# Kernel tuning notes

Measured on AMD Instinct MI355X. Metric: run time of the kernel, lower is better.

The kernel has to match this reference:

```python
import jax, jax.numpy as jnp
import numpy as np

D_STATE = 16
D_CONV = 4


def _ln_cf(x, w, b, eps=1e-6):
    # channels_first LayerNorm over dim 1 of (B,C,H,W)
    u = x.mean(1, keepdims=True)
    s = ((x - u) ** 2).mean(1, keepdims=True)
    return w[:, None, None] * ((x - u) / jnp.sqrt(s + eps)) + b[:, None, None]


def _ln_last(x, w, b, eps=1e-5):
    u = x.mean(-1, keepdims=True)
    s = ((x - u) ** 2).mean(-1, keepdims=True)
    return (x - u) / jnp.sqrt(s + eps) * w + b


def _mamba(xn, Win, convw, convb, Wx, Wdt, bdt, Alog, Dp):
    # xn: (B, L, d_model); returns (B, L, d_inner) (out_proj is Identity in this module)
    B, L, _ = xn.shape
    di = Win.shape[0] // 2
    xz = xn @ Win.T                                   # (B,L,2*di), in_proj bias=False
    xc, z = xz[..., :di], xz[..., di:]
    # causal depthwise conv1d along L (pad left d_conv-1, slice == torch pad+trim)
    xt = jnp.pad(xc.transpose(0, 2, 1), ((0, 0), (0, 0), (D_CONV - 1, 0)))
    xt = jax.lax.conv_general_dilated(xt, convw[:, None, :], (1,), 'VALID',
                                      dimension_numbers=('NCH', 'OIH', 'NCH'),
                                      feature_group_count=di)
    xs = jax.nn.silu(xt + convb[None, :, None]).transpose(0, 2, 1)  # (B,L,di)
    dtr = Wdt.shape[1]
    x_dbl = xs @ Wx.T                                 # (B,L,dtr+2*ds)
    dt = x_dbl[..., :dtr]
    Bm = x_dbl[..., dtr:dtr + D_STATE]                # (B,L,ds)
    Cm = x_dbl[..., dtr + D_STATE:]                   # (B,L,ds)
    delta = jax.nn.softplus(dt @ Wdt.T + bdt)         # (B,L,di)
    A = -jnp.exp(Alog)                                # (di,ds)
    dA = jnp.exp(delta[..., None] * A)                # (B,L,di,ds)
    dBx = delta[..., None] * Bm[:, :, None, :] * xs[..., None]

    def step(h, ab):
        a, b2 = ab
        h = a * h + b2
        return h, h

    h0 = jnp.zeros((B, di, D_STATE), xn.dtype)
    _, hs = jax.lax.scan(step, h0, (dA.transpose(1, 0, 2, 3), dBx.transpose(1, 0, 2, 3)))
    y = jnp.einsum('lbds,bls->bld', hs, Cm) + xs * Dp
    return y * jax.nn.silu(z)


def _dwconv2d(u, k, dil):
    c = k.shape[0]
    return jax.lax.conv_general_dilated(u, k[:, None], (1, 1),
                                        [(dil, dil), (dil, dil)],
                                        rhs_dilation=(dil, dil),
                                        dimension_numbers=('NCHW', 'OIHW', 'NCHW'),
                                        feature_group_count=c)


def _block(x, gamma1, gamma2, ln1_w, ln1_b, mn_w, mn_b,
           f_Win, f_convw, f_convb, f_Wx, f_Wdt, f_bdt, f_Alog, f_D,
           b_Win, b_convw, b_convb, b_Wx, b_Wdt, b_bdt, b_Alog, b_D,
           Wout, msff_win, msff_dw1, msff_dw2, msff_dw3, msff_wout):
    B, C, H, W = x.shape
    L = H * W
    # --- BiPixelMambaLayer branch ---
    x1 = _ln_cf(x, ln1_w, ln1_b)                       # norm1 (channels_first)
    xf = x1.reshape(B, C, L).transpose(0, 2, 1)        # (B,L,C)
    xn = _ln_last(xf, mn_w, mn_b)                      # inner nn.LayerNorm (eps=1e-5)
    yf = _mamba(xn, f_Win, f_convw, f_convb, f_Wx, f_Wdt, f_bdt, f_Alog, f_D)
    yb = _mamba(xn[:, ::-1], b_Win, b_convw, b_convb, b_Wx, b_Wdt, b_bdt, b_Alog, b_D)
    yo = (yf + yb[:, ::-1]) @ Wout.T                   # shared out_proj (bias=False)
    x = x + gamma1[:, None, None] * (yo.transpose(0, 2, 1).reshape(B, C, H, W) + x1)
    # --- MSFF branch (norm1 reused) ---
    inp = x
    xm = _ln_cf(x, ln1_w, ln1_b)
    h = jnp.einsum('oc,bchw->bohw', msff_win, xm)      # project_in (1x1x1 conv, depth=1)
    hid = msff_dw1.shape[0]
    h1 = _dwconv2d(h[:, :hid], msff_dw1, 1)            # Conv3d 3x3x3 w/ depth=1 == 2D center slice
    h2 = _dwconv2d(h[:, hid:2 * hid], msff_dw2, 2)
    h3 = _dwconv2d(h[:, 2 * hid:], msff_dw3, 3)
    g = jax.nn.gelu(h1, approximate=False) * h2 * h3
    xm = jnp.einsum('oc,bchw->bohw', msff_wout, g)     # project_out
    return inp + gamma2[:, None, None] * xm


def setup_inputs() -> dict:
    key = jax.random.key(0)
    ks = jax.random.split(key, 40)
    dim, di, dtr, ds, hid, Bn, H, W = 96, 192, 6, 16, 192, 2, 64, 64
    r = lambda i, shape, s=0.05: jax.random.normal(ks[i], shape, jnp.float32) * s
    inp = {
        'x': r(0, (Bn, dim, H, W), 1.0),
        'gamma1': r(1, (dim,), 0.1), 'gamma2': r(2, (dim,), 0.1),
        'ln1_w': 1.0 + r(3, (dim,), 0.1), 'ln1_b': r(4, (dim,), 0.1),
        'mn_w': 1.0 + r(5, (dim,), 0.1), 'mn_b': r(6, (dim,), 0.1),
    }
    i = 7
    for p in ('f_', 'b_'):
        inp[p + 'Win'] = r(i, (2 * di, dim)); i += 1
        inp[p + 'convw'] = r(i, (di, D_CONV), 0.2); i += 1
        inp[p + 'convb'] = r(i, (di,), 0.1); i += 1
        inp[p + 'Wx'] = r(i, (dtr + 2 * ds, di)); i += 1
        inp[p + 'Wdt'] = r(i, (di, dtr), 0.1); i += 1
        inp[p + 'bdt'] = r(i, (di,), 0.1); i += 1
        inp[p + 'Alog'] = jax.random.uniform(ks[i], (di, ds), jnp.float32, 0.0, 2.5); i += 1
        inp[p + 'D'] = r(i, (di,), 0.5); i += 1
    inp['Wout'] = r(i, (dim, di)); i += 1
    inp['msff_win'] = r(i, (3 * hid, dim)); i += 1
    inp['msff_dw1'] = r(i, (hid, 3, 3), 0.2); i += 1
    inp['msff_dw2'] = r(i, (hid, 3, 3), 0.2); i += 1
    inp['msff_dw3'] = r(i, (hid, 3, 3), 0.2); i += 1
    inp['msff_wout'] = r(i, (dim, hid)); i += 1
    return inp


def reference(x, gamma1, gamma2, ln1_w, ln1_b, mn_w, mn_b,
              f_Win, f_convw, f_convb, f_Wx, f_Wdt, f_bdt, f_Alog, f_D,
              b_Win, b_convw, b_convb, b_Wx, b_Wdt, b_bdt, b_Alog, b_D,
              Wout, msff_win, msff_dw1, msff_dw2, msff_dw3, msff_wout):
    return _block(x, gamma1, gamma2, ln1_w, ln1_b, mn_w, mn_b,
                  f_Win, f_convw, f_convb, f_Wx, f_Wdt, f_bdt, f_Alog, f_D,
                  b_Win, b_convw, b_convb, b_Wx, b_Wdt, b_bdt, b_Alog, b_D,
                  Wout, msff_win, msff_dw1, msff_dw2, msff_dw3, msff_wout)
```

## Files before the change

### kernel.cpp

```cpp
#include <hip/hip_runtime.h>
#include <hip/hip_bf16.h>
#include <math.h>

typedef __hip_bfloat16 bf16;
typedef _Float16 f16;
typedef f16  f16x8  __attribute__((ext_vector_type(8)));
typedef short short8 __attribute__((ext_vector_type(8)));
typedef unsigned short ushort8 __attribute__((ext_vector_type(8)));
typedef float floatx4 __attribute__((ext_vector_type(4)));

#define L_SEQ 4096
#define BATCH 2
#define DIM   96
#define DI    192
#define DS    16
#define HID   192
#define NPOS  (BATCH * L_SEQ)
#define NCH   256
#define CHUNK 16
#define GRP   16
#define NGRP  (NCH / GRP)
#define NREC  (2 * BATCH * DI)
#define LDBL  40
#define PLANE (4 * NCH * DI * 8)
#define LOG2E 1.44269504088896f
#define TP    32

__device__ __forceinline__ float silu_f(float x) { return x / (1.f + __expf(-x)); }
__device__ __forceinline__ float softplus_f(float x) {
    return fmaxf(x, 0.f) + __logf(1.f + __expf(-fabsf(x)));
}
__device__ __forceinline__ float b2f(bf16 v) { return __bfloat162float(v); }
__device__ __forceinline__ float us2f(unsigned short u) {
    union { unsigned int i; float f; } cv; cv.i = ((unsigned int)u) << 16; return cv.f;
}

__global__ void k_ln12_prep(const float* __restrict__ x,
                            const float* __restrict__ ln1w, const float* __restrict__ ln1b,
                            const float* __restrict__ mnw,  const float* __restrict__ mnb,
                            bf16* __restrict__ XNbf,
                            const float* __restrict__ fWin, const float* __restrict__ bWin,
                            const float* __restrict__ fWx,  const float* __restrict__ bWx,
                            const float* __restrict__ Wout, const float* __restrict__ mwin,
                            const float* __restrict__ mwout,
                            const float* __restrict__ fAlog, const float* __restrict__ bAlog,
                            const float* __restrict__ mdw1, const float* __restrict__ mdw2,
                            const float* __restrict__ mdw3,
                            bf16* __restrict__ war, float* __restrict__ a2tab,
                            float* __restrict__ mdwt) {
    __shared__ float xt[DIM][TP + 1];
    __shared__ float rs[8][TP], rss[8][TP];
    __shared__ float uu[TP], rr[TP];
    if (blockIdx.x >= NPOS / TP) {
        int i = (blockIdx.x - NPOS / TP) * 256 + threadIdx.x;
        if (i < 180480) {
            float v;
            if (i < 36864)        v = fWin[i];
            else if (i < 73728)   v = bWin[i - 36864];
            else if (i < 81024)   v = fWx[i - 73728];
            else if (i < 88320)   v = bWx[i - 81024];
            else if (i < 106752)  v = Wout[i - 88320];
            else if (i < 162048)  v = mwin[i - 106752];
            else                  v = mwout[i - 162048];
            war[i] = __float2bfloat16(v);
        } else if (i < 186624) {
            int j = i - 180480;
            int dirq = j / 3072, rem = j % 3072;
            const float* al = dirq ? bAlog : fAlog;
            a2tab[j] = -__expf(al[rem]) * LOG2E;
        } else if (i < 191808) {
            int j = i - 186624;
            int cv = j / 1728, rem = j % 1728;
            int tap = rem / 192, c = rem % 192;
            const float* src = (cv == 0) ? mdw1 : (cv == 1) ? mdw2 : mdw3;
            mdwt[j] = src[c * 9 + tap];
        }
        return;
    }
    int p0 = blockIdx.x * TP;
    int b = p0 >> 12, l0 = p0 & (L_SEQ - 1);
    int t = threadIdx.x;
    int tg = t >> 5, li = t & 31;

    for (int idx = t; idx < DIM * TP; idx += 256) {
        int c = idx >> 5, q = idx & 31;
        xt[c][q] = x[((size_t)(b * DIM + c)) * L_SEQ + l0 + q];
    }
    __syncthreads();
    {
        float s = 0.f, ss = 0.f;
        for (int c = tg; c < DIM; c += 8) { float v = xt[c][li]; s += v; ss += v * v; }
        rs[tg][li] = s; rss[tg][li] = ss;
    }
    __syncthreads();
    if (t < TP) {
        float s = 0.f, ss = 0.f;
#pragma unroll
        for (int g = 0; g < 8; g++) { s += rs[g][t]; ss += rss[g][t]; }
        float u = s / DIM;
        uu[t] = u; rr[t] = rsqrtf(ss / DIM - u * u + 1e-6f);
    }
    __syncthreads();
    {
        float u = uu[li], r = rr[li];
        float s2 = 0.f, ss2 = 0.f;
        for (int c = tg; c < DIM; c += 8) {
            float tv = ln1w[c] * (xt[c][li] - u) * r + ln1b[c];
            xt[c][li] = tv;
            s2 += tv; ss2 += tv * tv;
        }
        rs[tg][li] = s2; rss[tg][li] = ss2;
    }
    __syncthreads();
    if (t < TP) {
        float s = 0.f, ss = 0.f;
#pragma unroll
        for (int g = 0; g < 8; g++) { s += rs[g][t]; ss += rss[g][t]; }
        float u = s / DIM;
        uu[t] = u; rr[t] = rsqrtf(ss / DIM - u * u + 1e-5f);
    }
    __syncthreads();
    for (int idx = t; idx < DIM * TP; idx += 256) {
        int q = idx / DIM, c = idx % DIM;
        XNbf[(size_t)(p0 + q) * DIM + c] =
            __float2bfloat16((xt[c][q] - uu[q]) * rr[q] * mnw[c] + mnb[c]);
    }
}

__global__ void mfma_nt_dir(const bf16* __restrict__ A0, const bf16* __restrict__ A1,
                            const bf16* __restrict__ W0, const bf16* __restrict__ W1,
                            void* __restrict__ C0, void* __restrict__ C1,
                            int M, int N, int K, int ldc, int pad6, int obf) {
    int z = blockIdx.z;
    const bf16* A = z ? A1 : A0;
    const bf16* W = z ? W1 : W0;
    void* C = z ? C1 : C0;
    int wave = threadIdx.x >> 6, lane = threadIdx.x & 63;
    int m0 = blockIdx.x * 64 + wave * 16;
    int n0 = blockIdx.y * 64;
    int lm = lane & 15, quad = lane >> 4;
    const short* Ap = (const short*)A + (size_t)(m0 + lm) * K + quad * 8;
    const short* Wp = (const short*)W;
    floatx4 acc[4];
#pragma unroll
    for (int t = 0; t < 4; t++) acc[t] = (floatx4){0.f, 0.f, 0.f, 0.f};
    for (int k0 = 0; k0 < K; k0 += 32) {
        short8 a = *(const short8*)(Ap + k0);
#pragma unroll
        for (int t = 0; t < 4; t++) {
            int n = n0 + t * 16 + lm;
            short8 b = (n < N) ? *(const short8*)(Wp + (size_t)n * K + k0 + quad * 8)
                               : (short8){0,0,0,0,0,0,0,0};
            acc[t] = __builtin_amdgcn_mfma_f32_16x16x32_bf16(a, b, acc[t], 0, 0, 0);
        }
    }
#pragma unroll
    for (int t = 0; t < 4; t++) {
        int n = n0 + t * 16 + lm;
        if (n < N) {
            int nn = (pad6 && n >= 6) ? n + 2 : n;
#pragma unroll
            for (int r = 0; r < 4; r++) {
                int m = m0 + quad * 4 + r;
                if (obf) ((bf16*)C)[(size_t)m * ldc + nn] = __float2bfloat16(acc[t][r]);
                else     ((float*)C)[(size_t)m * ldc + nn] = acc[t][r];
            }
        }
    }
}

__global__ void k_conv_dbl(const bf16* __restrict__ XZF, const bf16* __restrict__ XZB,
                           const float* __restrict__ fw, const float* __restrict__ fb,
                           const float* __restrict__ bw, const float* __restrict__ bb,
                           const bf16* __restrict__ fWxB, const bf16* __restrict__ bWxB,
                           float* __restrict__ DBLF, float* __restrict__ DBLB,
                           bf16* __restrict__ XSF, bf16* __restrict__ XSB) {
    __shared__ __align__(16) unsigned short xs_t[64][200];
    int dirb = blockIdx.y;
    int p0 = blockIdx.x * 64;
    const bf16* XZ = dirb ? XZB : XZF;
    const float* cw = dirb ? bw : fw;
    const float* cb = dirb ? bb : fb;
    bf16* XS = dirb ? XSB : XSF;

    for (int u = threadIdx.x; u < 64 * 24; u += 256) {
        int dg = u % 24, pl = u / 24;
        int p = p0 + pl;
        int b = p >> 12, l = p & (L_SEQ - 1);
        int d0 = dg * 8;
        float4 w[8];
#pragma unroll
        for (int j = 0; j < 8; j++) w[j] = *(const float4*)(cw + (d0 + j) * 4);
        float acc[8];
#pragma unroll
        for (int j = 0; j < 8; j++) acc[j] = cb[d0 + j];
#pragma unroll
        for (int k = 0; k < 4; k++) {
            int ls = dirb ? (l + 3 - k) : (l - 3 + k);
            if (ls >= 0 && ls < L_SEQ) {
                ushort8 xv = *(const ushort8*)((const unsigned short*)XZ +
                               ((size_t)(b * L_SEQ + ls)) * 384 + d0);
#pragma unroll
                for (int j = 0; j < 8; j++) {
                    float wk = (k == 0) ? w[j].x : (k == 1) ? w[j].y : (k == 2) ? w[j].z : w[j].w;
                    acc[j] += wk * us2f(xv[j]);
                }
            }
        }
        ushort8 ov;
#pragma unroll
        for (int j = 0; j < 8; j++) {
            bf16 tv = __float2bfloat16(silu_f(acc[j]));
            ov[j] = *(unsigned short*)&tv;
        }
        *(ushort8*)((unsigned short*)XS + (size_t)p * DI + d0) = ov;
        *(ushort8*)&xs_t[pl][d0] = ov;
    }
    __syncthreads();
    int t = threadIdx.x;
    int w = t >> 6, lane = t & 63;
    int lm = lane & 15, quad = lane >> 4;
    const bf16* Wx = dirb ? bWxB : fWxB;
    float* DBL = dirb ? DBLB : DBLF;
    floatx4 acc[3];
#pragma unroll
    for (int tt = 0; tt < 3; tt++) acc[tt] = (floatx4){0.f, 0.f, 0.f, 0.f};
    const unsigned short* ar = &xs_t[w * 16 + lm][0];
#pragma unroll
    for (int k = 0; k < 6; k++) {
        int k0 = k * 32 + quad * 8;
        short8 a = *(const short8*)(ar + k0);
#pragma unroll
        for (int tt = 0; tt < 3; tt++) {
            int n = tt * 16 + lm;
            short8 bq = (n < 38) ? *(const short8*)((const short*)Wx + n * 192 + k0)
                                 : (short8){0,0,0,0,0,0,0,0};
            acc[tt] = __builtin_amdgcn_mfma_f32_16x16x32_bf16(a, bq, acc[tt], 0, 0, 0);
        }
    }
#pragma unroll
    for (int tt = 0; tt < 3; tt++) {
        int n = tt * 16 + lm;
        if (n < 38) {
            int nn = (n >= 6) ? n + 2 : n;
#pragma unroll
            for (int r = 0; r < 4; r++) {
                int m = p0 + w * 16 + quad * 4 + r;
                DBL[(size_t)m * LDBL + nn] = acc[tt][r];
            }
        }
    }
}

__global__ void k_scan_p1g(const float* __restrict__ DBLF, const float* __restrict__ DBLB,
                           const bf16* __restrict__ XSF,  const bf16* __restrict__ XSB,
                           const float* __restrict__ fWdt, const float* __restrict__ fbdt,
                           const float* __restrict__ bWdt, const float* __restrict__ bbdt,
                           const float* __restrict__ a2tab,
                           f16* __restrict__ Pexc, f16* __restrict__ Qexc,
                           float* __restrict__ Pg, float* __restrict__ Qg) {
    __shared__ f16x8 Pl[2][GRP][16];
    __shared__ f16x8 Ql[2][GRP][16];
    int dsl = blockIdx.x, grp = blockIdx.y, dirb = blockIdx.z;
    int t = threadIdx.x;
    int chunk = t >> 4, dl = t & 15;
    int d = dsl * 16 + dl;
    int b = dirb & 1, dir = dirb >> 1;
    int gc = grp * GRP + chunk;

    const float* DBL = dir ? DBLB : DBLF;
    const bf16*  XS  = dir ? XSB  : XSF;
    const float* wdt = (dir ? bWdt : fWdt) + d * 6;
    float bdtv = (dir ? bbdt : fbdt)[d];

    float wd[6];
#pragma unroll
    for (int r = 0; r < 6; r++) wd[r] = wdt[r];
    const float* a2p = a2tab + (dir * DI + d) * 16;
    float A2[16], h[16];
#pragma unroll
    for (int v = 0; v < 4; v++) {
        float4 a2v = *(const float4*)(a2p + 4 * v);
        A2[4*v] = a2v.x; A2[4*v+1] = a2v.y; A2[4*v+2] = a2v.z; A2[4*v+3] = a2v.w;
    }
#pragma unroll
    for (int s = 0; s < 16; s++) h[s] = 0.f;

    int l = dir ? (L_SEQ - 1 - gc * CHUNK) : gc * CHUNK;
    int stp = dir ? -1 : 1;
    float sumdel = 0.f;

    for (int i = 0; i < CHUNK; i++) {
        size_t p = (size_t)b * L_SEQ + l;
        const float* row = DBL + p * LDBL;
        float dtv = bdtv;
#pragma unroll
        for (int r = 0; r < 6; r++) dtv += row[r] * wd[r];
        float del = softplus_f(dtv);
        float xs  = b2f(XS[p * DI + d]);
        const float4* bm = (const float4*)(row + 8);
        float4 B0 = bm[0], B1 = bm[1], B2 = bm[2], B3 = bm[3];
        float Bm[16] = {B0.x,B0.y,B0.z,B0.w, B1.x,B1.y,B1.z,B1.w,
                        B2.x,B2.y,B2.z,B2.w, B3.x,B3.y,B3.z,B3.w};
        float dx = del * xs;
        sumdel += del;
#pragma unroll
        for (int s = 0; s < 16; s++) {
            float dA = exp2f(del * A2[s]);
            h[s] = dA * h[s] + dx * Bm[s];
        }
        l += stp;
    }
    {
        f16x8 p0, p1, q0, q1;
#pragma unroll
        for (int j = 0; j < 8; j++) {
            q0[j] = (f16)h[j];
            q1[j] = (f16)h[8 + j];
            p0[j] = (f16)exp2f(A2[j] * sumdel);
            p1[j] = (f16)exp2f(A2[8 + j] * sumdel);
        }
        Pl[0][chunk][dl] = p0; Pl[1][chunk][dl] = p1;
        Ql[0][chunk][dl] = q0; Ql[1][chunk][dl] = q1;
    }
    __syncthreads();

    {
        int s  = t & 15, dl2 = t >> 4;
        int s8 = s >> 3, sl = s & 7;
        f16* Pp = (f16*)&Pl[s8][0][dl2];
        f16* Qp = (f16*)&Ql[s8][0][dl2];
        float runP = 1.f, runQ = 0.f;
#pragma unroll
        for (int c = 0; c < GRP; c++) {
            float pv = (float)Pp[c * 128 + sl];
            float qv = (float)Qp[c * 128 + sl];
            Pp[c * 128 + sl] = (f16)runP;
            Qp[c * 128 + sl] = (f16)runQ;
            runQ = pv * runQ + qv;
            runP *= pv;
        }
        int d2 = dsl * 16 + dl2;
        size_t gidx = (((size_t)(dirb * NGRP + grp)) * DI + d2) * 16 + s;
        Pg[gidx] = runP;
        Qg[gidx] = runQ;
    }
    __syncthreads();

    {
        size_t base = ((size_t)(dirb * NCH + gc) * DI + d) * 8;
        *(f16x8*)(Pexc + base)         = Pl[0][chunk][dl];
        *(f16x8*)(Pexc + PLANE + base) = Pl[1][chunk][dl];
        *(f16x8*)(Qexc + base)         = Ql[0][chunk][dl];
        *(f16x8*)(Qexc + PLANE + base) = Ql[1][chunk][dl];
    }
}

__global__ void k_scan_p3g(const float* __restrict__ DBLF, const float* __restrict__ DBLB,
                           const bf16* __restrict__ XSF,  const bf16* __restrict__ XSB,
                           const bf16* __restrict__ XZF,  const bf16* __restrict__ XZB,
                           const float* __restrict__ fWdt, const float* __restrict__ fbdt,
                           const float* __restrict__ bWdt, const float* __restrict__ bbdt,
                           const float* __restrict__ a2tab,
                           const float* __restrict__ fD,    const float* __restrict__ bD,
                           const f16* __restrict__ Pexc, const f16* __restrict__ Qexc,
                           const float* __restrict__ Pg, const float* __restrict__ Qg,
                           bf16* __restrict__ YSF, bf16* __restrict__ YSB) {
    __shared__ float qx[16][17];
    int dsl = blockIdx.x, grp = blockIdx.y, dirb = blockIdx.z;
    int t = threadIdx.x;
    {
        int dl = t >> 4, s = t & 15;
        int d2 = dsl * 16 + dl;
        float runQ = 0.f;
        for (int g = 0; g < grp; g++) {
            size_t i = (((size_t)(dirb * NGRP + g)) * DI + d2) * 16 + s;
            runQ = Pg[i] * runQ + Qg[i];
        }
        qx[dl][s] = runQ;
    }
    __syncthreads();

    int chunk = t >> 4, dl = t & 15;
    int d = dsl * 16 + dl;
    int gc = grp * GRP + chunk;
    int b = dirb & 1, dir = dirb >> 1;

    const float* DBL = dir ? DBLB : DBLF;
    const bf16*  XS  = dir ? XSB  : XSF;
    const bf16*  XZ  = dir ? XZB  : XZF;
    const float* wdt = (dir ? bWdt : fWdt) + d * 6;
    float bdtv = (dir ? bbdt : fbdt)[d];
    float Dp = dir ? bD[d] : fD[d];
    bf16* Y = dir ? YSB : YSF;

    float wd[6];
#pragma unroll
    for (int r = 0; r < 6; r++) wd[r] = wdt[r];
    const float* a2p = a2tab + (dir * DI + d) * 16;
    float A2[16], h[16];
#pragma unroll
    for (int v = 0; v < 4; v++) {
        float4 a2v = *(const float4*)(a2p + 4 * v);
        A2[4*v] = a2v.x; A2[4*v+1] = a2v.y; A2[4*v+2] = a2v.z; A2[4*v+3] = a2v.w;
    }
    {
        size_t base = ((size_t)(dirb * NCH + gc) * DI + d) * 8;
        f16x8 pe0 = *(const f16x8*)(Pexc + base);
        f16x8 pe1 = *(const f16x8*)(Pexc + PLANE + base);
        f16x8 qe0 = *(const f16x8*)(Qexc + base);
        f16x8 qe1 = *(const f16x8*)(Qexc + PLANE + base);
#pragma unroll
        for (int j = 0; j < 8; j++) {
            h[j]     = (float)pe0[j] * qx[dl][j]     + (float)qe0[j];
            h[8 + j] = (float)pe1[j] * qx[dl][8 + j] + (float)qe1[j];
        }
    }

    int l = dir ? (L_SEQ - 1 - gc * CHUNK) : gc * CHUNK;
    int stp = dir ? -1 : 1;

    for (int i = 0; i < CHUNK; i++) {
        size_t p = (size_t)b * L_SEQ + l;
        const float* row = DBL + p * LDBL;
        float dtv = bdtv;
#pragma unroll
        for (int r = 0; r < 6; r++) dtv += row[r] * wd[r];
        float del = softplus_f(dtv);
        float xs  = b2f(XS[p * DI + d]);
        float z   = b2f(XZ[p * 384 + 192 + d]);
        const float4* bm = (const float4*)(row + 8);
        float4 B0 = bm[0], B1 = bm[1], B2 = bm[2], B3 = bm[3];
        float4 C0 = bm[4], C1 = bm[5], C2 = bm[6], C3 = bm[7];
        float Bm[16] = {B0.x,B0.y,B0.z,B0.w, B1.x,B1.y,B1.z,B1.w,
                        B2.x,B2.y,B2.z,B2.w, B3.x,B3.y,B3.z,B3.w};
        float Cm[16] = {C0.x,C0.y,C0.z,C0.w, C1.x,C1.y,C1.z,C1.w,
                        C2.x,C2.y,C2.z,C2.w, C3.x,C3.y,C3.z,C3.w};
        float dx = del * xs;
        float pr = 0.f;
#pragma unroll
        for (int s = 0; s < 16; s++) {
            float dA = exp2f(del * A2[s]);
            h[s] = dA * h[s] + dx * Bm[s];
            pr += h[s] * Cm[s];
        }
        Y[p * DI + d] = __float2bfloat16((pr + xs * Dp) * silu_f(z));
        l += stp;
    }
}

__global__ void k_out_mid(const bf16* __restrict__ Y1, const bf16* __restrict__ Y2,
                          const bf16* __restrict__ W,
                          const float* __restrict__ x, const float* __restrict__ gamma1,
                          const float* __restrict__ ln1w, const float* __restrict__ ln1b,
                          const bf16* __restrict__ mwinB,
                          float* __restrict__ XMID, bf16* __restrict__ H) {
    __shared__ float yt[DIM][TP + 1];
    __shared__ float xt[DIM][TP + 1];
    __shared__ float rs[8][TP], rss[8][TP];
    __shared__ float uu[TP], rr[TP];
    __shared__ __align__(16) unsigned short xmt[TP][104];
    int p0 = blockIdx.x * TP;
    int b = p0 >> 12, l0 = p0 & (L_SEQ - 1);
    int t = threadIdx.x;
    int tg = t >> 5, li = t & 31;

    {
        int w = t >> 6, lane = t & 63;
        int lm = lane & 15, quad = lane >> 4;
        int mh = w & 1, nb = (w >> 1) * 3;
        const short* A1p = (const short*)Y1 + (size_t)(p0 + mh * 16 + lm) * 192 + quad * 8;
        const short* A2p = (const short*)Y2 + (size_t)(p0 + mh * 16 + lm) * 192 + quad * 8;
        const short* Wp  = (const short*)W;
        floatx4 acc[3];
#pragma unroll
        for (int tt = 0; tt < 3; tt++) acc[tt] = (floatx4){0.f, 0.f, 0.f, 0.f};
#pragma unroll
        for (int k = 0; k < 6; k++) {
            int k0 = k * 32;
            short8 a1 = *(const short8*)(A1p + k0);
            short8 a2 = *(const short8*)(A2p + k0);
#pragma unroll
            for (int tt = 0; tt < 3; tt++) {
                int n = (nb + tt) * 16 + lm;
                short8 bq = *(const short8*)(Wp + (size_t)n * 192 + k0 + quad * 8);
                acc[tt] = __builtin_amdgcn_mfma_f32_16x16x32_bf16(a1, bq, acc[tt], 0, 0, 0);
                acc[tt] = __builtin_amdgcn_mfma_f32_16x16x32_bf16(a2, bq, acc[tt], 0, 0, 0);
            }
        }
#pragma unroll
        for (int tt = 0; tt < 3; tt++) {
            int c = (nb + tt) * 16 + lm;
#pragma unroll
            for (int r = 0; r < 4; r++)
                yt[c][mh * 16 + quad * 4 + r] = acc[tt][r];
        }
    }
    for (int idx = t; idx < DIM * TP; idx += 256) {
        int c = idx >> 5, q = idx & 31;
        xt[c][q] = x[((size_t)(b * DIM + c)) * L_SEQ + l0 + q];
    }
    __syncthreads();
    {
        float s = 0.f, ss = 0.f;
        for (int c = tg; c < DIM; c += 8) { float v = xt[c][li]; s += v; ss += v * v; }
        rs[tg][li] = s; rss[tg][li] = ss;
    }
    __syncthreads();
    if (t < TP) {
        float s = 0.f, ss = 0.f;
#pragma unroll
        for (int g = 0; g < 8; g++) { s += rs[g][t]; ss += rss[g][t]; }
        float u = s / DIM;
        uu[t] = u; rr[t] = rsqrtf(ss / DIM - u * u + 1e-6f);
    }
    __syncthreads();
    {
        float u = uu[li], r = rr[li];
        float s = 0.f, ss = 0.f;
        for (int c = tg; c < DIM; c += 8) {
            float xv = xt[c][li];
            float x1 = ln1w[c] * (xv - u) * r + ln1b[c];
            float v = xv + gamma1[c] * (yt[c][li] + x1);
            XMID[((size_t)(b * DIM + c)) * L_SEQ + l0 + li] = v;
            xt[c][li] = v;
            s += v; ss += v * v;
        }
        rs[tg][li] = s; rss[tg][li] = ss;
    }
    __syncthreads();
    if (t < TP) {
        float s = 0.f, ss = 0.f;
#pragma unroll
        for (int g = 0; g < 8; g++) { s += rs[g][t]; ss += rss[g][t]; }
        float u = s / DIM;
        uu[t] = u; rr[t] = rsqrtf(ss / DIM - u * u + 1e-6f);
    }
    __syncthreads();
    for (int idx = t; idx < DIM * TP; idx += 256) {
        int q = idx / DIM, c = idx % DIM;
        bf16 tv = __float2bfloat16(ln1w[c] * (xt[c][q] - uu[q]) * rr[q] + ln1b[c]);
        xmt[q][c] = *(unsigned short*)&tv;
    }
    __syncthreads();
    {
        int w = t >> 6, lane = t & 63;
        int lm = lane & 15, quad = lane >> 4;
        int mh = w & 1, ng = w >> 1;
        const unsigned short* ar = &xmt[mh * 16 + lm][0];
        short8 a[3];
#pragma unroll
        for (int k = 0; k < 3; k++)
            a[k] = *(const short8*)(ar + k * 32 + quad * 8);
        const short* Wp = (const short*)mwinB;
#pragma unroll
        for (int tt = 0; tt < 18; tt++) {
            int n = (ng * 18 + tt) * 16 + lm;
            floatx4 acc = (floatx4){0.f, 0.f, 0.f, 0.f};
#pragma unroll
            for (int k = 0; k < 3; k++) {
                short8 bq = *(const short8*)(Wp + (size_t)n * 96 + k * 32 + quad * 8);
                acc = __builtin_amdgcn_mfma_f32_16x16x32_bf16(a[k], bq, acc, 0, 0, 0);
            }
#pragma unroll
            for (int r = 0; r < 4; r++) {
                int m = p0 + mh * 16 + quad * 4 + r;
                H[(size_t)m * 576 + n] = __float2bfloat16(acc[r]);
            }
        }
    }
}

__global__ void k_msff_outres(const bf16* __restrict__ H, const float* __restrict__ mdwt,
                              const bf16* __restrict__ mwoutB,
                              const float* __restrict__ XMID, const float* __restrict__ gamma2,
                              float* __restrict__ out) {
    __shared__ __align__(16) unsigned short gt[32][200];
    int p0 = blockIdx.x * 32;
    int t = threadIdx.x;
    const unsigned short* Hu = (const unsigned short*)H;

    for (int u = t; u < 32 * 24; u += 256) {
        int cg = u % 24, pl = u / 24;
        int p = p0 + pl;
        int c0 = cg * 8;
        int b = p >> 12, l = p & (L_SEQ - 1);
        int y = l >> 6, xc = l & 63;
        float a1[8] = {}, a2[8] = {}, a3[8] = {};
#pragma unroll
        for (int ky = 0; ky < 3; ky++) {
#pragma unroll
            for (int kx = 0; kx < 3; kx++) {
                int tap = ky * 3 + kx;
                {
                    int y1 = y + (ky - 1), x1 = xc + (kx - 1);
                    if (y1 >= 0 && y1 < 64 && x1 >= 0 && x1 < 64) {
                        float4 w0 = *(const float4*)(mdwt + tap * 192 + c0);
                        float4 w1 = *(const float4*)(mdwt + tap * 192 + c0 + 4);
                        ushort8 hv = *(const ushort8*)(Hu +
                            ((size_t)(b * L_SEQ + y1 * 64 + x1)) * 576 + c0);
                        float wv[8] = {w0.x,w0.y,w0.z,w0.w, w1.x,w1.y,w1.z,w1.w};
#pragma unroll
                        for (int j = 0; j < 8; j++) a1[j] += wv[j] * us2f(hv[j]);
                    }
                }
                {
                    int y2 = y + (ky - 1) * 2, x2 = xc + (kx - 1) * 2;
                    if (y2 >= 0 && y2 < 64 && x2 >= 0 && x2 < 64) {
                        float4 w0 = *(const float4*)(mdwt + (9 + tap) * 192 + c0);
                        float4 w1 = *(const float4*)(mdwt + (9 + tap) * 192 + c0 + 4);
                        ushort8 hv = *(const ushort8*)(Hu +
                            ((size_t)(b * L_SEQ + y2 * 64 + x2)) * 576 + 192 + c0);
                        float wv[8] = {w0.x,w0.y,w0.z,w0.w, w1.x,w1.y,w1.z,w1.w};
#pragma unroll
                        for (int j = 0; j < 8; j++) a2[j] += wv[j] * us2f(hv[j]);
                    }
                }
                {
                    int y3 = y + (ky - 1) * 3, x3 = xc + (kx - 1) * 3;
                    if (y3 >= 0 && y3 < 64 && x3 >= 0 && x3 < 64) {
                        float4 w0 = *(const float4*)(mdwt + (18 + tap) * 192 + c0);
                        float4 w1 = *(const float4*)(mdwt + (18 + tap) * 192 + c0 + 4);
                        ushort8 hv = *(const ushort8*)(Hu +
                            ((size_t)(b * L_SEQ + y3 * 64 + x3)) * 576 + 384 + c0);
                        float wv[8] = {w0.x,w0.y,w0.z,w0.w, w1.x,w1.y,w1.z,w1.w};
#pragma unroll
                        for (int j = 0; j < 8; j++) a3[j] += wv[j] * us2f(hv[j]);
                    }
                }
            }
        }
        ushort8 ov;
#pragma unroll
        for (int j = 0; j < 8; j++) {
            float ge = 0.5f * a1[j] * (1.f + erff(a1[j] * 0.70710678118f));
            bf16 tv = __float2bfloat16(ge * a2[j] * a3[j]);
            ov[j] = *(unsigned short*)&tv;
        }
        *(ushort8*)&gt[pl][c0] = ov;
    }
    __syncthreads();
    int w = t >> 6, lane = t & 63;
    int lm = lane & 15, quad = lane >> 4;
    int nt = w & 1, mb = (w >> 1) * 3;
    floatx4 acc[3];
#pragma unroll
    for (int tt = 0; tt < 3; tt++) acc[tt] = (floatx4){0.f, 0.f, 0.f, 0.f};
    const unsigned short* br = &gt[nt * 16 + lm][0];
#pragma unroll
    for (int k = 0; k < 6; k++) {
        int k0 = k * 32 + quad * 8;
        short8 bq = *(const short8*)(br + k0);
#pragma unroll
        for (int tt = 0; tt < 3; tt++) {
            int m = (mb + tt) * 16 + lm;
            short8 a = *(const short8*)((const short*)mwoutB + m * 192 + k0);
            acc[tt] = __builtin_amdgcn_mfma_f32_16x16x32_bf16(a, bq, acc[tt], 0, 0, 0);
        }
    }
    int b = p0 >> 12, l0 = p0 & (L_SEQ - 1);
#pragma unroll
    for (int tt = 0; tt < 3; tt++) {
#pragma unroll
        for (int r = 0; r < 4; r++) {
            int m = (mb + tt) * 16 + quad * 4 + r;
            size_t idx = ((size_t)(b * DIM + m)) * L_SEQ + l0 + nt * 16 + lm;
            out[idx] = XMID[idx] + gamma2[m] * acc[tt][r];
        }
    }
}

extern "C" void kernel_launch(void* const* d_in, const int* in_sizes, int n_in,
                              void* d_out, int out_size, void* d_ws, size_t ws_size,
                              hipStream_t stream) {
    const float* x      = (const float*)d_in[0];
    const float* gamma1 = (const float*)d_in[1];
    const float* gamma2 = (const float*)d_in[2];
    const float* ln1w   = (const float*)d_in[3];
    const float* ln1b   = (const float*)d_in[4];
    const float* mnw    = (const float*)d_in[5];
    const float* mnb    = (const float*)d_in[6];
    const float* fWin   = (const float*)d_in[7];
    const float* fconvw = (const float*)d_in[8];
    const float* fconvb = (const float*)d_in[9];
    const float* fWx    = (const float*)d_in[10];
    const float* fWdt   = (const float*)d_in[11];
    const float* fbdt   = (const float*)d_in[12];
    const float* fAlog  = (const float*)d_in[13];
    const float* fD     = (const float*)d_in[14];
    const float* bWin   = (const float*)d_in[15];
    const float* bconvw = (const float*)d_in[16];
    const float* bconvb = (const float*)d_in[17];
    const float* bWx    = (const float*)d_in[18];
    const float* bWdt   = (const float*)d_in[19];
    const float* bbdt   = (const float*)d_in[20];
    const float* bAlog  = (const float*)d_in[21];
    const float* bD     = (const float*)d_in[22];
    const float* Wout   = (const float*)d_in[23];
    const float* mwin   = (const float*)d_in[24];
    const float* mdw1   = (const float*)d_in[25];
    const float* mdw2   = (const float*)d_in[26];
    const float* mdw3   = (const float*)d_in[27];
    const float* mwout  = (const float*)d_in[28];
    float* out = (float*)d_out;

    float* ws = (float*)d_ws;
    bf16*  XNbf  = (bf16*)(ws);
    bf16*  XZF   = (bf16*)(ws + 393216);
    bf16*  XZB   = (bf16*)(ws + 1966080);
    bf16*  XSF   = (bf16*)(ws + 3538944);
    bf16*  XSB   = (bf16*)(ws + 4325376);
    float* DBLF  = ws + 5111808;
    float* DBLB  = ws + 5439488;
    f16*   Ph    = (f16*)(ws + 5767168);
    f16*   Qh    = (f16*)(ws + 8912896);
    bf16*  YSFbf = (bf16*)(ws + 12058624);
    bf16*  YSBbf = (bf16*)(ws + 12845056);
    float* XMID  = ws + 14417920;
    bf16*  Hcl   = (bf16*)(ws + 15597568);
    bf16*  WAR   = (bf16*)(ws + 18743296);
    float* A2tab = ws + 18833536;
    float* MDWT  = ws + 18839680;
    float* Pgb   = ws + 18844864;
    float* Qgb   = ws + 19041472;

    const bf16* fWinB  = WAR;
    const bf16* bWinB  = WAR + 36864;
    const bf16* fWxB   = WAR + 73728;
    const bf16* bWxB   = WAR + 81024;
    const bf16* WoutB  = WAR + 88320;
    const bf16* mwinB  = WAR + 106752;
    const bf16* mwoutB = WAR + 162048;

    k_ln12_prep<<<NPOS / TP + 750, 256, 0, stream>>>(
        x, ln1w, ln1b, mnw, mnb, XNbf,
        fWin, bWin, fWx, bWx, Wout, mwin, mwout,
        fAlog, bAlog, mdw1, mdw2, mdw3, WAR, A2tab, MDWT);
    mfma_nt_dir<<<dim3(128, 6, 2), 256, 0, stream>>>(XNbf, XNbf, fWinB, bWinB,
                                                     XZF, XZB, NPOS, 384, DIM, 384, 0, 1);
    k_conv_dbl<<<dim3(NPOS / 64, 2), 256, 0, stream>>>(
        XZF, XZB, fconvw, fconvb, bconvw, bconvb,
        fWxB, bWxB, DBLF, DBLB, XSF, XSB);
    k_scan_p1g<<<dim3(DI / 16, NGRP, 4), 256, 0, stream>>>(
        DBLF, DBLB, XSF, XSB, fWdt, fbdt, bWdt, bbdt,
        A2tab, Ph, Qh, Pgb, Qgb);
    k_scan_p3g<<<dim3(DI / 16, NGRP, 4), 256, 0, stream>>>(
        DBLF, DBLB, XSF, XSB, XZF, XZB,
        fWdt, fbdt, bWdt, bbdt, A2tab, fD, bD,
        Ph, Qh, Pgb, Qgb, YSFbf, YSBbf);
    k_out_mid<<<NPOS / TP, 256, 0, stream>>>(
        YSFbf, YSBbf, WoutB, x, gamma1, ln1w, ln1b, mwinB, XMID, Hcl);
    k_msff_outres<<<NPOS / 32, 256, 0, stream>>>(Hcl, MDWT, mwoutB, XMID, gamma2, out);
}
```

Measured before the change: 264.5 us.

## Fuse two scan passes into one cooperative kernel with grid sync

Merges the chunk-summary scan pass and the output scan pass into a single cooperative kernel that uses a grid-wide sync between them. The per-chunk exclusive P/Q prefixes stay in shared memory instead of being written to and re-read from global memory. This removes one kernel launch and the f16 exchange buffers. In exchange it adds a grid barrier, and it relies on all 768 blocks being co-resident, which is why launch bounds of 3 blocks per CU are set.

```diff
diff --git a/kernel.cpp b/kernel.cpp
--- a/kernel.cpp
+++ b/kernel.cpp
@@ -1,6 +1,9 @@
 #include <hip/hip_runtime.h>
 #include <hip/hip_bf16.h>
+#include <hip/hip_cooperative_groups.h>
 #include <math.h>
+
+namespace cg = cooperative_groups;
 
 typedef __hip_bfloat16 bf16;
 typedef _Float16 f16;
@@ -20,9 +23,7 @@
 #define CHUNK 16
 #define GRP   16
 #define NGRP  (NCH / GRP)
-#define NREC  (2 * BATCH * DI)
 #define LDBL  40
-#define PLANE (4 * NCH * DI * 8)
 #define LOG2E 1.44269504088896f
 #define TP    32
 
@@ -252,15 +253,19 @@
     }
 }
 
-__global__ void k_scan_p1g(const float* __restrict__ DBLF, const float* __restrict__ DBLB,
-                           const bf16* __restrict__ XSF,  const bf16* __restrict__ XSB,
-                           const float* __restrict__ fWdt, const float* __restrict__ fbdt,
-                           const float* __restrict__ bWdt, const float* __restrict__ bbdt,
-                           const float* __restrict__ a2tab,
-                           f16* __restrict__ Pexc, f16* __restrict__ Qexc,
-                           float* __restrict__ Pg, float* __restrict__ Qg) {
+__global__ void __launch_bounds__(256, 3)
+k_scan_fused(const float* __restrict__ DBLF, const float* __restrict__ DBLB,
+             const bf16* __restrict__ XSF,  const bf16* __restrict__ XSB,
+             const bf16* __restrict__ XZF,  const bf16* __restrict__ XZB,
+             const float* __restrict__ fWdt, const float* __restrict__ fbdt,
+             const float* __restrict__ bWdt, const float* __restrict__ bbdt,
+             const float* __restrict__ a2tab,
+             const float* __restrict__ fD,    const float* __restrict__ bD,
+             float* __restrict__ Pg, float* __restrict__ Qg,
+             bf16* __restrict__ YSF, bf16* __restrict__ YSB) {
     __shared__ f16x8 Pl[2][GRP][16];
     __shared__ f16x8 Ql[2][GRP][16];
+    __shared__ float qx[16][17];
     int dsl = blockIdx.x, grp = blockIdx.y, dirb = blockIdx.z;
     int t = threadIdx.x;
     int chunk = t >> 4, dl = t & 15;
@@ -270,8 +275,11 @@
 
     const float* DBL = dir ? DBLB : DBLF;
     const bf16*  XS  = dir ? XSB  : XSF;
+    const bf16*  XZ  = dir ? XZB  : XZF;
     const float* wdt = (dir ? bWdt : fWdt) + d * 6;
     float bdtv = (dir ? bbdt : fbdt)[d];
+    float Dp = dir ? bD[d] : fD[d];
+    bf16* Y = dir ? YSB : YSF;
 
     float wd[6];
 #pragma unroll
@@ -286,32 +294,33 @@
 #pragma unroll
     for (int s = 0; s < 16; s++) h[s] = 0.f;
 
-    int l = dir ? (L_SEQ - 1 - gc * CHUNK) : gc * CHUNK;
+    int l0 = dir ? (L_SEQ - 1 - gc * CHUNK) : gc * CHUNK;
     int stp = dir ? -1 : 1;
     float sumdel = 0.f;
 
-    for (int i = 0; i < CHUNK; i++) {
-        size_t p = (size_t)b * L_SEQ + l;
-        const float* row = DBL + p * LDBL;
-        float dtv = bdtv;
-#pragma unroll
-        for (int r = 0; r < 6; r++) dtv += row[r] * wd[r];
-        float del = softplus_f(dtv);
-        float xs  = b2f(XS[p * DI + d]);
-        const float4* bm = (const float4*)(row + 8);
-        float4 B0 = bm[0], B1 = bm[1], B2 = bm[2], B3 = bm[3];
-        float Bm[16] = {B0.x,B0.y,B0.z,B0.w, B1.x,B1.y,B1.z,B1.w,
-                        B2.x,B2.y,B2.z,B2.w, B3.x,B3.y,B3.z,B3.w};
-        float dx = del * xs;
-        sumdel += del;
-#pragma unroll
-        for (int s = 0; s < 16; s++) {
-            float dA = exp2f(del * A2[s]);
-            h[s] = dA * h[s] + dx * Bm[s];
-        }
-        l += stp;
-    }
-    {
+    {
+        int l = l0;
+        for (int i = 0; i < CHUNK; i++) {
+            size_t p = (size_t)b * L_SEQ + l;
+            const float* row = DBL + p * LDBL;
+            float dtv = bdtv;
+#pragma unroll
+            for (int r = 0; r < 6; r++) dtv += row[r] * wd[r];
+            float del = softplus_f(dtv);
+            float xs  = b2f(XS[p * DI + d]);
+            const float4* bm = (const float4*)(row + 8);
+            float4 B0 = bm[0], B1 = bm[1], B2 = bm[2], B3 = bm[3];
+            float Bm[16] = {B0.x,B0.y,B0.z,B0.w, B1.x,B1.y,B1.z,B1.w,
+                            B2.x,B2.y,B2.z,B2.w, B3.x,B3.y,B3.z,B3.w};
+            float dx = del * xs;
+            sumdel += del;
+#pragma unroll
+            for (int s = 0; s < 16; s++) {
+                float dA = exp2f(del * A2[s]);
+                h[s] = dA * h[s] + dx * Bm[s];
+            }
+            l += stp;
+        }
         f16x8 p0, p1, q0, q1;
 #pragma unroll
         for (int j = 0; j < 8; j++) {
@@ -345,107 +354,61 @@
         Pg[gidx] = runP;
         Qg[gidx] = runQ;
     }
-    __syncthreads();
-
-    {
-        size_t base = ((size_t)(dirb * NCH + gc) * DI + d) * 8;
-        *(f16x8*)(Pexc + base)         = Pl[0][chunk][dl];
-        *(f16x8*)(Pexc + PLANE + base) = Pl[1][chunk][dl];
-        *(f16x8*)(Qexc + base)         = Ql[0][chunk][dl];
-        *(f16x8*)(Qexc + PLANE + base) = Ql[1][chunk][dl];
-    }
-}
-
-__global__ void k_scan_p3g(const float* __restrict__ DBLF, const float* __restrict__ DBLB,
-                           const bf16* __restrict__ XSF,  const bf16* __restrict__ XSB,
-                           const bf16* __restrict__ XZF,  const bf16* __restrict__ XZB,
-                           const float* __restrict__ fWdt, const float* __restrict__ fbdt,
-                           const float* __restrict__ bWdt, const float* __restrict__ bbdt,
-                           const float* __restrict__ a2tab,
-                           const float* __restrict__ fD,    const float* __restrict__ bD,
-                           const f16* __restrict__ Pexc, const f16* __restrict__ Qexc,
-                           const float* __restrict__ Pg, const float* __restrict__ Qg,
-                           bf16* __restrict__ YSF, bf16* __restrict__ YSB) {
-    __shared__ float qx[16][17];
-    int dsl = blockIdx.x, grp = blockIdx.y, dirb = blockIdx.z;
-    int t = threadIdx.x;
-    {
-        int dl = t >> 4, s = t & 15;
-        int d2 = dsl * 16 + dl;
+    __threadfence();
+    cg::this_grid().sync();
+
+    {
+        int dl2 = t >> 4, s = t & 15;
+        int d2 = dsl * 16 + dl2;
         float runQ = 0.f;
         for (int g = 0; g < grp; g++) {
             size_t i = (((size_t)(dirb * NGRP + g)) * DI + d2) * 16 + s;
             runQ = Pg[i] * runQ + Qg[i];
         }
-        qx[dl][s] = runQ;
-    }
-    __syncthreads();
-
-    int chunk = t >> 4, dl = t & 15;
-    int d = dsl * 16 + dl;
-    int gc = grp * GRP + chunk;
-    int b = dirb & 1, dir = dirb >> 1;
-
-    const float* DBL = dir ? DBLB : DBLF;
-    const bf16*  XS  = dir ? XSB  : XSF;
-    const bf16*  XZ  = dir ? XZB  : XZF;
-    const float* wdt = (dir ? bWdt : fWdt) + d * 6;
-    float bdtv = (dir ? bbdt : fbdt)[d];
-    float Dp = dir ? bD[d] : fD[d];
-    bf16* Y = dir ? YSB : YSF;
-
-    float wd[6];
-#pragma unroll
-    for (int r = 0; r < 6; r++) wd[r] = wdt[r];
-    const float* a2p = a2tab + (dir * DI + d) * 16;
-    float A2[16], h[16];
-#pragma unroll
-    for (int v = 0; v < 4; v++) {
-        float4 a2v = *(const float4*)(a2p + 4 * v);
-        A2[4*v] = a2v.x; A2[4*v+1] = a2v.y; A2[4*v+2] = a2v.z; A2[4*v+3] = a2v.w;
-    }
-    {
-        size_t base = ((size_t)(dirb * NCH + gc) * DI + d) * 8;
-        f16x8 pe0 = *(const f16x8*)(Pexc + base);
-        f16x8 pe1 = *(const f16x8*)(Pexc + PLANE + base);
-        f16x8 qe0 = *(const f16x8*)(Qexc + base);
-        f16x8 qe1 = *(const f16x8*)(Qexc + PLANE + base);
+        qx[dl2][s] = runQ;
+    }
+    __syncthreads();
+
+    {
+        f16x8 pe0 = Pl[0][chunk][dl];
+        f16x8 pe1 = Pl[1][chunk][dl];
+        f16x8 qe0 = Ql[0][chunk][dl];
+        f16x8 qe1 = Ql[1][chunk][dl];
 #pragma unroll
         for (int j = 0; j < 8; j++) {
             h[j]     = (float)pe0[j] * qx[dl][j]     + (float)qe0[j];
             h[8 + j] = (float)pe1[j] * qx[dl][8 + j] + (float)qe1[j];
         }
     }
-
-    int l = dir ? (L_SEQ - 1 - gc * CHUNK) : gc * CHUNK;
-    int stp = dir ? -1 : 1;
-
-    for (int i = 0; i < CHUNK; i++) {
-        size_t p = (size_t)b * L_SEQ + l;
-        const float* row = DBL + p * LDBL;
-        float dtv = bdtv;
-#pragma unroll
-        for (int r = 0; r < 6; r++) dtv += row[r] * wd[r];
-        float del = softplus_f(dtv);
-        float xs  = b2f(XS[p * DI + d]);
-        float z   = b2f(XZ[p * 384 + 192 + d]);
-        const float4* bm = (const float4*)(row + 8);
-        float4 B0 = bm[0], B1 = bm[1], B2 = bm[2], B3 = bm[3];
-        float4 C0 = bm[4], C1 = bm[5], C2 = bm[6], C3 = bm[7];
-        float Bm[16] = {B0.x,B0.y,B0.z,B0.w, B1.x,B1.y,B1.z,B1.w,
-                        B2.x,B2.y,B2.z,B2.w, B3.x,B3.y,B3.z,B3.w};
-        float Cm[16] = {C0.x,C0.y,C0.z,C0.w, C1.x,C1.y,C1.z,C1.w,
-                        C2.x,C2.y,C2.z,C2.w, C3.x,C3.y,C3.z,C3.w};
-        float dx = del * xs;
-        float pr = 0.f;
-#pragma unroll
-        for (int s = 0; s < 16; s++) {
-            float dA = exp2f(del * A2[s]);
-            h[s] = dA * h[s] + dx * Bm[s];
-            pr += h[s] * Cm[s];
-        }
-        Y[p * DI + d] = __float2bfloat16((pr + xs * Dp) * silu_f(z));
-        l += stp;
+    {
+        int l = l0;
+        for (int i = 0; i < CHUNK; i++) {
+            size_t p = (size_t)b * L_SEQ + l;
+            const float* row = DBL + p * LDBL;
+            float dtv = bdtv;
+#pragma unroll
+            for (int r = 0; r < 6; r++) dtv += row[r] * wd[r];
+            float del = softplus_f(dtv);
+            float xs  = b2f(XS[p * DI + d]);
+            float z   = b2f(XZ[p * 384 + 192 + d]);
+            const float4* bm = (const float4*)(row + 8);
+            float4 B0 = bm[0], B1 = bm[1], B2 = bm[2], B3 = bm[3];
+            float4 C0 = bm[4], C1 = bm[5], C2 = bm[6], C3 = bm[7];
+            float Bm[16] = {B0.x,B0.y,B0.z,B0.w, B1.x,B1.y,B1.z,B1.w,
+                            B2.x,B2.y,B2.z,B2.w, B3.x,B3.y,B3.z,B3.w};
+            float Cm[16] = {C0.x,C0.y,C0.z,C0.w, C1.x,C1.y,C1.z,C1.w,
+                            C2.x,C2.y,C2.z,C2.w, C3.x,C3.y,C3.z,C3.w};
+            float dx = del * xs;
+            float pr = 0.f;
+#pragma unroll
+            for (int s = 0; s < 16; s++) {
+                float dA = exp2f(del * A2[s]);
+                h[s] = dA * h[s] + dx * Bm[s];
+                pr += h[s] * Cm[s];
+            }
+            Y[p * DI + d] = __float2bfloat16((pr + xs * Dp) * silu_f(z));
+            l += stp;
+        }
     }
 }
 
@@ -712,8 +675,6 @@
     bf16*  XSB   = (bf16*)(ws + 4325376);
     float* DBLF  = ws + 5111808;
     float* DBLB  = ws + 5439488;
-    f16*   Ph    = (f16*)(ws + 5767168);
-    f16*   Qh    = (f16*)(ws + 8912896);
     bf16*  YSFbf = (bf16*)(ws + 12058624);
     bf16*  YSBbf = (bf16*)(ws + 12845056);
     float* XMID  = ws + 14417920;
@@ -741,13 +702,18 @@
     k_conv_dbl<<<dim3(NPOS / 64, 2), 256, 0, stream>>>(
         XZF, XZB, fconvw, fconvb, bconvw, bconvb,
         fWxB, bWxB, DBLF, DBLB, XSF, XSB);
-    k_scan_p1g<<<dim3(DI / 16, NGRP, 4), 256, 0, stream>>>(
-        DBLF, DBLB, XSF, XSB, fWdt, fbdt, bWdt, bbdt,
-        A2tab, Ph, Qh, Pgb, Qgb);
-    k_scan_p3g<<<dim3(DI / 16, NGRP, 4), 256, 0, stream>>>(
-        DBLF, DBLB, XSF, XSB, XZF, XZB,
-        fWdt, fbdt, bWdt, bbdt, A2tab, fD, bD,
-        Ph, Qh, Pgb, Qgb, YSFbf, YSBbf);
+    {
+        void* args[] = {
+            (void*)&DBLF, (void*)&DBLB, (void*)&XSF, (void*)&XSB,
+            (void*)&XZF, (void*)&XZB,
+            (void*)&fWdt, (void*)&fbdt, (void*)&bWdt, (void*)&bbdt,
+            (void*)&A2tab, (void*)&fD, (void*)&bD,
+            (void*)&Pgb, (void*)&Qgb, (void*)&YSFbf, (void*)&YSBbf
+        };
+        hipLaunchCooperativeKernel((const void*)k_scan_fused,
+                                   dim3(DI / 16, NGRP, 4), dim3(256),
+                                   args, 0, stream);
+    }
     k_out_mid<<<NPOS / TP, 256, 0, stream>>>(
         YSFbf, YSBbf, WoutB, x, gamma1, ln1w, ln1b, mwinB, XMID, Hcl);
     k_msff_outres<<<NPOS / 32, 256, 0, stream>>>(Hcl, MDWT, mwoutB, XMID, gamma2, out);
```

New measurement: 410.8 us. 1.55x slower.
